# Kernel tuning notes

Hardware: AMD Instinct MI355X
Metric: run time of the kernel (lower is better)

The kernel has to match this reference:

```python
import jax, jax.numpy as jnp
import numpy as np

_INF = -1e30
EPS = 1e-8


def _masked_max(v, mask, axis, keepdims=False):
    return jnp.max(jnp.where(mask == 0, _INF, v), axis=axis, keepdims=keepdims)


def _masked_mean(v, mask, axis, keepdims=False):
    s = jnp.sum(jnp.where(mask == 0, 0.0, v), axis=axis, keepdims=keepdims)
    cnt = jnp.sum(jnp.broadcast_to(mask, v.shape), axis=axis, keepdims=keepdims)
    return s / jnp.clip(cnt, EPS, None)


def _masked_softmax(v, mask):
    return jax.nn.softmax(jnp.where(mask == 0, _INF, v), axis=-1)


def _cos(a, b, axis):
    num = jnp.sum(a * b, axis=axis)
    na = jnp.maximum(jnp.sqrt(jnp.sum(a * a, axis=axis)), EPS)
    nb = jnp.maximum(jnp.sqrt(jnp.sum(b * b, axis=axis)), EPS)
    return num / (na * nb)


def _pairwise_cos(c1, c2):
    # c1:[B,L1,H] c2:[B,L2,H] -> [B,L1,L2]
    dots = jnp.einsum('bih,bjh->bij', c1, c2)
    n1 = jnp.maximum(jnp.linalg.norm(c1, axis=-1), EPS)
    n2 = jnp.maximum(jnp.linalg.norm(c2, axis=-1), EPS)
    return dots / (n1[:, :, None] * n2[:, None, :])


def _mpm(v1, v2, w):
    # v1:[B,L,H], v2:[B,L or 1,H], w:[P,H]
    single = _cos(v1, v2, axis=2)[:, :, None]              # [B,L,1]
    wv1 = w[None, None] * v1[:, :, None, :]                # [B,L,P,H]
    wv2 = w[None, None] * v2[:, :, None, :]                # [B,Lv,P,H]
    multi = _cos(wv1, wv2, axis=3)                         # [B,L,P]
    return single, multi


def _mpm_pairwise(c1, c2, w):
    # w:[P,H] -> cosine [B,L1,L2,P]
    wv1 = w[None, :, None, :] * c1[:, None, :, :]          # [B,P,L1,H]
    wv2 = w[None, :, None, :] * c2[:, None, :, :]          # [B,P,L2,H]
    n1 = jnp.linalg.norm(wv1, axis=3, keepdims=True)       # [B,P,L1,1]
    n2 = jnp.linalg.norm(wv2, axis=3, keepdims=True)       # [B,P,L2,1]
    mul = jnp.einsum('bpih,bpjh->bpij', wv1, wv2)
    denom = jnp.clip(n1 * jnp.swapaxes(n2, 2, 3), EPS, None)
    return jnp.transpose(mul / denom, (0, 2, 3, 1))        # [B,L1,L2,P]


def _bimpm(context_1, mask_1, context_2, mask_2, w_ff, w_fb, w_mp, w_att, w_matt):
    B = context_1.shape[0]
    len1 = jnp.sum(mask_1, axis=1).astype(jnp.int32)
    len2 = jnp.sum(mask_2, axis=1).astype(jnp.int32)
    c1 = context_1 * mask_1[:, :, None]
    c2 = context_2 * mask_2[:, :, None]

    cos_sim = _pairwise_cos(c1, c2)                        # [B,L1,L2]
    m2r = mask_2[:, None, :]
    m1r = mask_1[:, None, :]
    cmax1 = _masked_max(cos_sim, m2r, 2, True)
    cmean1 = _masked_mean(cos_sim, m2r, 2, True)
    cos_t = jnp.swapaxes(cos_sim, 1, 2)
    cmax2 = _masked_max(cos_t, m1r, 2, True)
    cmean2 = _masked_mean(cos_t, m1r, 2, True)

    lp1 = jnp.clip(len1 - 1, 0, None)
    lp2 = jnp.clip(len2 - 1, 0, None)
    c1_fl = c1[jnp.arange(B), lp1][:, None, :]             # [B,1,H]
    c2_fl = c2[jnp.arange(B), lp2][:, None, :]
    c1_bl = c1[:, 0:1, :]
    c2_bl = c2[:, 0:1, :]

    mv1_ff = _mpm(c1, c2_fl, w_ff)
    mv2_ff = _mpm(c2, c1_fl, w_ff)
    mv1_bf = _mpm(c1, c2_bl, w_fb)
    mv2_bf = _mpm(c2, c1_bl, w_fb)

    mm = _mpm_pairwise(c1, c2, w_mp)                       # [B,L1,L2,P]
    mv1_max = _masked_max(mm, mask_2[:, None, :, None], 2)
    mv1_mean = _masked_mean(mm, mask_2[:, None, :, None], 2)
    mm_t = jnp.transpose(mm, (0, 2, 1, 3))
    mv2_max = _masked_max(mm_t, mask_1[:, None, :, None], 2)
    mv2_mean = _masked_mean(mm_t, mask_1[:, None, :, None], 2)

    att_2 = c2[:, None, :, :] * cos_sim[:, :, :, None]     # [B,L1,L2,H]
    att_1 = c1[:, :, None, :] * cos_sim[:, :, :, None]     # [B,L1,L2,H]
    att_mean_2 = _masked_softmax(att_2.sum(axis=2), mask_1[:, :, None])  # [B,L1,H]
    att_mean_1 = _masked_softmax(att_1.sum(axis=1), mask_2[:, :, None])  # [B,L2,H]
    mv1_am = _mpm(c1, att_mean_2, w_att)
    mv2_am = _mpm(c2, att_mean_1, w_att)

    att_max_2 = _masked_max(att_2, mask_2[:, None, :, None], 2)          # [B,L1,H]
    att_max_1 = _masked_max(jnp.transpose(att_1, (0, 2, 1, 3)), mask_1[:, None, :, None], 2)  # [B,L2,H]
    mv1_amx = _mpm(c1, att_max_2, w_matt)
    mv2_amx = _mpm(c2, att_max_1, w_matt)

    mv1 = jnp.concatenate([cmax1, cmean1, *mv1_ff, *mv1_bf, mv1_max, mv1_mean, *mv1_am, *mv1_amx], axis=-1)
    mv2 = jnp.concatenate([cmax2, cmean2, *mv2_ff, *mv2_bf, mv2_max, mv2_mean, *mv2_am, *mv2_amx], axis=-1)
    return jnp.concatenate([mv1, mv2], axis=1)             # [B, L1+L2, 102]


def setup_inputs() -> dict:
    key = jax.random.key(0)
    B, L, H, P = 8, 128, 768, 16
    ks = jax.random.split(key, 8)
    context_1 = jax.random.normal(ks[0], (B, L, H), dtype=jnp.float32)
    context_2 = jax.random.normal(ks[1], (B, L, H), dtype=jnp.float32)
    len1 = jax.random.randint(ks[2], (B,), L // 2, L + 1)
    len2 = jax.random.randint(ks[3], (B,), L // 2, L + 1)
    ar = jnp.arange(L)
    mask_1 = (ar[None, :] < len1[:, None]).astype(jnp.float32)
    mask_2 = (ar[None, :] < len2[:, None]).astype(jnp.float32)
    scale = np.sqrt(2.0 / H).astype(np.float32)
    w_ff = jax.random.normal(ks[4], (P, H), dtype=jnp.float32) * scale
    w_fb = jax.random.normal(ks[5], (P, H), dtype=jnp.float32) * scale
    w_mp = jax.random.normal(ks[6], (P, H), dtype=jnp.float32) * scale
    kk = jax.random.split(ks[7], 2)
    w_att = jax.random.normal(kk[0], (P, H), dtype=jnp.float32) * scale
    w_matt = jax.random.normal(kk[1], (P, H), dtype=jnp.float32) * scale
    return {"context_1": context_1, "mask_1": mask_1, "context_2": context_2, "mask_2": mask_2,
            "w_ff": w_ff, "w_fb": w_fb, "w_mp": w_mp, "w_att": w_att, "w_matt": w_matt}


def reference(context_1, mask_1, context_2, mask_2, w_ff, w_fb, w_mp, w_att, w_matt):
    return _bimpm(context_1, mask_1, context_2, mask_2, w_ff, w_fb, w_mp, w_att, w_matt)
```

## Files before the change

### kernel.cpp

```cpp
#include <hip/hip_runtime.h>

#define Bn 8
#define Ln 128
#define Hn 768
#define Pn 16
#define Dn 102
#define EPSF 1e-8f
#define NINF -1e30f

typedef __attribute__((ext_vector_type(8))) short bfrag8;
typedef __attribute__((ext_vector_type(4))) float f32x4;
union FragU { unsigned u[4]; bfrag8 v; };

#define MFMA16(A,B,C) __builtin_amdgcn_mfma_f32_16x16x32_bf16((A),(B),(C),0,0,0)

__device__ __forceinline__ float wred_sum(float v){
#pragma unroll
  for(int o=32;o>=1;o>>=1) v += __shfl_xor(v,o);
  return v;
}
__device__ __forceinline__ float wred_max(float v){
#pragma unroll
  for(int o=32;o>=1;o>>=1) v = fmaxf(v,__shfl_xor(v,o));
  return v;
}
__device__ __forceinline__ float qred_sum(float v){
  v += __shfl_xor(v,16);
  v += __shfl_xor(v,32);
  return v;
}

__device__ __forceinline__ void split8(const float* x, FragU& H, FragU& L){
  float r[8];
#pragma unroll
  for(int q=0;q<8;q++){
    unsigned hb = __float_as_uint(x[q]) & 0xffff0000u;
    r[q] = x[q] - __uint_as_float(hb);
  }
#pragma unroll
  for(int q=0;q<4;q++){
    H.u[q] = __builtin_amdgcn_perm(__float_as_uint(x[2*q+1]), __float_as_uint(x[2*q]), 0x07060302u);
    L.u[q] = __builtin_amdgcn_perm(__float_as_uint(r[2*q+1]), __float_as_uint(r[2*q]), 0x07060302u);
  }
}

#define GLD_LDS(gp, lp) __builtin_amdgcn_global_load_lds( \
    (const __attribute__((address_space(1))) void*)(gp), \
    (__attribute__((address_space(3))) void*)(lp), 16, 0, 0)

constexpr size_t SZ_MAT   = (size_t)Bn*Ln*Hn;
constexpr size_t OFF_C1F  = 0;
constexpr size_t OFF_C2F  = OFF_C1F + SZ_MAT;
constexpr size_t OFF_COS  = OFF_C2F + SZ_MAT;
constexpr size_t OFF_N1   = OFF_COS + (size_t)Bn*Ln*Ln;
constexpr size_t OFF_N2   = OFF_N1 + (size_t)Bn*Ln;
constexpr size_t OFF_WN   = OFF_N2 + (size_t)Bn*Ln;
constexpr size_t OFF_W2T  = OFF_WN + (size_t)2*5*Bn*Pn*Ln;
constexpr size_t OFF_MVMAX  = OFF_W2T + (size_t)5*Hn*Pn;
constexpr size_t OFF_MVMEAN = OFF_MVMAX + (size_t)2*Bn*Ln*Pn;
constexpr size_t OFF_PART   = OFF_MVMEAN + (size_t)2*Bn*Ln*Pn;
constexpr size_t OFF_LENS   = OFF_PART + (size_t)Bn*Ln*Pn*32*2;
constexpr size_t OFF_C2H    = OFF_LENS + 32;
constexpr size_t OFF_C2L    = OFF_C2H + (size_t)Bn*12*128*64/2;
constexpr size_t OFF_W2F    = OFF_C2L + (size_t)Bn*12*128*64/2;
constexpr size_t OFF_W2B    = OFF_W2F + 12288;

__device__ __forceinline__ size_t wnIdx(int side,int X,int b,int p,int i){
  return ((((size_t)side*5 + X)*Bn + b)*Pn + p)*Ln + i;
}

__global__ __launch_bounds__(256) void k_prep(
    const float* __restrict__ m1, const float* __restrict__ m2,
    const float* __restrict__ wff, const float* __restrict__ wfb,
    const float* __restrict__ wmp, const float* __restrict__ watt,
    const float* __restrict__ wmatt,
    float* __restrict__ W2T, float* __restrict__ W2F, float* __restrict__ W2B,
    int* __restrict__ lens){
  int t = threadIdx.x;
  const float* srcs[5] = {wff,wfb,wmp,watt,wmatt};
  if(blockIdx.x < 8){
    int b = blockIdx.x;
    __shared__ int cnt[2];
    if(t<2) cnt[t]=0;
    __syncthreads();
    if(t<Ln){
      if(m1[b*Ln+t]>0.5f) atomicAdd(&cnt[0],1);
      if(m2[b*Ln+t]>0.5f) atomicAdd(&cnt[1],1);
    }
    __syncthreads();
    if(t==0){
      lens[b]=cnt[0]; lens[8+b]=cnt[1];
      lens[16+b]=max(cnt[0]-1,0); lens[24+b]=max(cnt[1]-1,0);
    }
  } else if(blockIdx.x < 248){
    int idx = (blockIdx.x-8)*256 + t;
    int X = idx/(Pn*Hn);
    int r = idx%(Pn*Hn);
    int h = r/Pn, p = r%Pn;
    float w = srcs[X][p*Hn+h];
    W2T[idx] = w*w;
  } else if(blockIdx.x < 296){
    int idx = (blockIdx.x-248)*256 + t;
    int ksg = idx>>9;
    int r   = idx&511;
    int half= r>>8;
    int li  = (r>>2)&63;
    int e4  = r&3;
    int h = ksg*32 + half*16 + ((li>>4)<<2) + e4;
    int p = li&15;
    float w = wmp[p*Hn+h];
    W2F[idx] = w*w;
  } else {
    int idx = (blockIdx.x-296)*256 + t;
    int X   = idx/12288;
    int r   = idx%12288;
    int hh4 = r>>8;
    int li  = (r>>2)&63;
    int e   = r&3;
    int h = (li>>4)*192 + hh4*4 + e;
    int p = li&15;
    float w = srcs[X][p*Hn+h];
    W2B[idx] = w*w;
  }
}

__global__ __launch_bounds__(256) void k_rows(
    const float* __restrict__ ctx1, const float* __restrict__ m1,
    const float* __restrict__ ctx2, const float* __restrict__ m2,
    const float* __restrict__ W2T,
    float* __restrict__ c1f, float* __restrict__ c2f,
    unsigned short* __restrict__ c2h, unsigned short* __restrict__ c2l,
    float* __restrict__ n1, float* __restrict__ n2, float* __restrict__ wn){
  const int i0 = blockIdx.x*4, b = blockIdx.y, side = blockIdx.z;
  const float* ctx = side? ctx2 : ctx1;
  const float* msk = side? m2 : m1;
  float* dst = side? c2f : c1f;
  float* nD  = side? n2 : n1;
  const int t = threadIdx.x, w = t>>6, l = t&63;

  __shared__ float red4[4][4];
  __shared__ float redX[4][4][16];
  __shared__ float mkS[4];

  if(t<4) mkS[t] = msk[b*Ln+i0+t];

#pragma unroll
  for(int r=0;r<4;r++){
    const int i = i0+r;
    const float mk = msk[b*Ln+i];
    const size_t base = ((size_t)(b*Ln+i))*Hn;
    float ss = 0.f;
#pragma unroll
    for(int k=0;k<3;k++){
      float x = ctx[base + t + 256*k]*mk;
      dst[base + t + 256*k] = x;
      ss = fmaf(x,x,ss);
      if(side==1){
        int h = t+256*k;
        int kc = h>>6, hw = h&63, u = hw>>2, e = hw&3;
        int pos = ((u ^ (i&15))<<2) + e;
        size_t o = ((size_t)(b*12+kc)*128 + i)*64 + pos;
        unsigned hb = __float_as_uint(x) & 0xffff0000u;
        float rem = x - __uint_as_float(hb);
        c2h[o] = (unsigned short)(hb>>16);
        c2l[o] = (unsigned short)(__float_as_uint(rem)>>16);
      }
    }
    ss = wred_sum(ss);
    if(l==0) red4[r][w]=ss;
  }
  __syncthreads();
  if(t<4) nD[b*Ln+i0+t] = sqrtf(fmaxf(red4[t][0]+red4[t][1]+red4[t][2]+red4[t][3],0.f));

  const int pq = t&3, hc = t>>2;
  const int h0 = hc*12;
  float v2r[4][12];
#pragma unroll
  for(int r=0;r<4;r++){
    const float mk = mkS[r];
    const float* src = ctx + ((size_t)(b*Ln+i0+r))*Hn + h0;
#pragma unroll
    for(int q=0;q<3;q++){
      float4 xv = *(const float4*)(src + q*4);
      v2r[r][q*4+0]=xv.x*xv.x*mk; v2r[r][q*4+1]=xv.y*xv.y*mk;
      v2r[r][q*4+2]=xv.z*xv.z*mk; v2r[r][q*4+3]=xv.w*xv.w*mk;
    }
  }
  for(int X=0;X<5;++X){
    float acc[4][4];
#pragma unroll
    for(int r=0;r<4;r++){ acc[r][0]=0.f; acc[r][1]=0.f; acc[r][2]=0.f; acc[r][3]=0.f; }
    const float* wb = W2T + (size_t)X*Hn*Pn + pq*4;
#pragma unroll
    for(int h=0;h<12;h++){
      float4 w4 = *(const float4*)(wb + (size_t)(h0+h)*Pn);
#pragma unroll
      for(int r=0;r<4;r++){
        acc[r][0]=fmaf(w4.x,v2r[r][h],acc[r][0]);
        acc[r][1]=fmaf(w4.y,v2r[r][h],acc[r][1]);
        acc[r][2]=fmaf(w4.z,v2r[r][h],acc[r][2]);
        acc[r][3]=fmaf(w4.w,v2r[r][h],acc[r][3]);
      }
    }
#pragma unroll
    for(int r=0;r<4;r++)
#pragma unroll
      for(int pi=0;pi<4;pi++){
        float v = acc[r][pi];
        v += __shfl_xor(v,4); v += __shfl_xor(v,8);
        v += __shfl_xor(v,16); v += __shfl_xor(v,32);
        acc[r][pi]=v;
      }
    if(l<4){
#pragma unroll
      for(int r=0;r<4;r++)
#pragma unroll
        for(int pi=0;pi<4;pi++) redX[w][l][r*4+pi]=acc[r][pi];
    }
    __syncthreads();
    if(t<64){
      int r = t>>4, p = t&15;
      int pqi = p>>2, pii = p&3;
      float s = redX[0][pqi][r*4+pii]+redX[1][pqi][r*4+pii]
               +redX[2][pqi][r*4+pii]+redX[3][pqi][r*4+pii];
      wn[wnIdx(side,X,b,p,i0+r)] = s;
    }
    __syncthreads();
  }
}

__global__ __launch_bounds__(512) void k_mm(
    const float* __restrict__ c1f,
    const unsigned short* __restrict__ c2h, const unsigned short* __restrict__ c2l,
    const float* __restrict__ W2F, const float* __restrict__ WN,
    const float* __restrict__ n1, const float* __restrict__ n2,
    const float* __restrict__ m1, const float* __restrict__ m2,
    const int* __restrict__ lens,
    float* __restrict__ cosM,
    float* __restrict__ mvmax, float* __restrict__ mvmean,
    float* __restrict__ part){
  const int b = blockIdx.x, ig = blockIdx.y, ibase = ig*4;
  const int t = threadIdx.x, l = t&63;
  const int wid = __builtin_amdgcn_readfirstlane(t>>6);
  const int jtp = wid&3, ihalf = wid>>2;
  const int p = l&15, g4 = l>>4;

  __shared__ __align__(16) unsigned short sB2h[2][128][64];
  __shared__ __align__(16) unsigned short sB2l[2][128][64];
  __shared__ __align__(16) float sw2[2][1024];
  __shared__ __align__(16) float sa[2][4][64];
  __shared__ float sm2s[Ln];
  __shared__ float red0[2][4][2][16][2];

  const size_t c2elem = (size_t)b*12*8192;

  {
#pragma unroll
    for(int k=0;k<2;k++){
      GLD_LDS((const char*)c2h + c2elem*2 + (2*wid+k)*1024 + l*16,
              (char*)&sB2h[0][0][0] + (2*wid+k)*1024);
      GLD_LDS((const char*)c2l + c2elem*2 + (2*wid+k)*1024 + l*16,
              (char*)&sB2l[0][0][0] + (2*wid+k)*1024);
    }
    if(wid>=4){
      int q = wid-4;
      GLD_LDS((const char*)W2F + q*1024 + l*16,
              (char*)&sw2[0][0] + q*1024);
    }
    if(t<Ln) sm2s[t] = m2[b*Ln+t];
    if(t<64){
      int row = t>>4, u = t&15;
      float4 av = *(const float4*)(c1f + ((size_t)(b*Ln+ibase+row))*Hn + u*4);
      *(float4*)&sa[0][row][(u ^ (row&3))<<2] = av;
    }
  }
  __syncthreads();

  f32x4 accE[2][2]; f32x4 accC[2];
#pragma unroll
  for(int q=0;q<2;q++){
    accC[q] = (f32x4){0.f,0.f,0.f,0.f};
#pragma unroll
    for(int ii=0;ii<2;ii++) accE[q][ii] = (f32x4){0.f,0.f,0.f,0.f};
  }

  for(int c=0; c<12; ++c){
    const int cur = c&1, nxt = cur^1;
    const bool more = (c+1<12);
    float4 aN;
    if(more){
      const size_t cb2 = (c2elem + (size_t)(c+1)*8192)*2;
#pragma unroll
      for(int k=0;k<2;k++){
        GLD_LDS((const char*)c2h + cb2 + (2*wid+k)*1024 + l*16,
                (char*)&sB2h[nxt][0][0] + (2*wid+k)*1024);
        GLD_LDS((const char*)c2l + cb2 + (2*wid+k)*1024 + l*16,
                (char*)&sB2l[nxt][0][0] + (2*wid+k)*1024);
      }
      if(wid>=4){
        int q = wid-4;
        GLD_LDS((const char*)W2F + (c+1)*4096 + q*1024 + l*16,
                (char*)&sw2[nxt][0] + q*1024);
      }
      if(t<64){
        int row = t>>4, u = t&15;
        aN = *(const float4*)(c1f + ((size_t)(b*Ln+ibase+row))*Hn + (c+1)*64 + u*4);
      }
    }
#pragma unroll
    for(int ks=0; ks<2; ++ks){
      f32x4 w20 = *(const f32x4*)&sw2[cur][(ks*2+0)*256 + (l<<2)];
      f32x4 w21 = *(const f32x4*)&sw2[cur][(ks*2+1)*256 + (l<<2)];
      FragU Bh[2], Bl[2];
#pragma unroll
      for(int q=0;q<2;q++){
        int jt = jtp + 4*q;
        int j  = jt*16 + p;
        const char* bh = (const char*)&sB2h[cur][0][0] + j*128;
        const char* bl = (const char*)&sB2l[cur][0][0] + j*128;
        int u1 = (ks*8 + g4)     ^ (j&15);
        int u2 = (ks*8 + 4 + g4) ^ (j&15);
        uint2 h0 = *(const uint2*)(bh + (u1<<3));
        uint2 h1 = *(const uint2*)(bh + (u2<<3));
        uint2 l0 = *(const uint2*)(bl + (u1<<3));
        uint2 l1 = *(const uint2*)(bl + (u2<<3));
        Bh[q].u[0]=h0.x; Bh[q].u[1]=h0.y; Bh[q].u[2]=h1.x; Bh[q].u[3]=h1.y;
        Bl[q].u[0]=l0.x; Bl[q].u[1]=l0.y; Bl[q].u[2]=l1.x; Bl[q].u[3]=l1.y;
      }
      if(ihalf==0){
        int ar = p&3;
        const float* sar = &sa[cur][ar][0];
        f32x4 a0 = *(const f32x4*)(sar + (((ks*8+g4)  ^ar)<<2));
        f32x4 a1 = *(const f32x4*)(sar + (((ks*8+4+g4)^ar)<<2));
        float xv[8] = {a0[0],a0[1],a0[2],a0[3], a1[0],a1[1],a1[2],a1[3]};
        FragU Ah, Al; split8(xv, Ah, Al);
#pragma unroll
        for(int q=0;q<2;q++){
          accC[q] = MFMA16(Bh[q].v, Ah.v, accC[q]);
          accC[q] = MFMA16(Bh[q].v, Al.v, accC[q]);
          accC[q] = MFMA16(Bl[q].v, Ah.v, accC[q]);
        }
      }
#pragma unroll
      for(int ii=0;ii<2;ii++){
        int row = ihalf*2+ii;
        const float* sar = &sa[cur][row][0];
        f32x4 a0 = *(const f32x4*)(sar + (((ks*8+g4)  ^(row&3))<<2));
        f32x4 a1 = *(const f32x4*)(sar + (((ks*8+4+g4)^(row&3))<<2));
        float xv[8] = {a0[0]*w20[0], a0[1]*w20[1], a0[2]*w20[2], a0[3]*w20[3],
                       a1[0]*w21[0], a1[1]*w21[1], a1[2]*w21[2], a1[3]*w21[3]};
        FragU Ah, Al; split8(xv, Ah, Al);
#pragma unroll
        for(int q=0;q<2;q++){
          accE[q][ii] = MFMA16(Bh[q].v, Ah.v, accE[q][ii]);
          accE[q][ii] = MFMA16(Bh[q].v, Al.v, accE[q][ii]);
          accE[q][ii] = MFMA16(Bl[q].v, Ah.v, accE[q][ii]);
        }
      }
    }
    if(more && t<64){
      int row = t>>4, u = t&15;
      *(float4*)&sa[nxt][row][(u ^ (row&3))<<2] = aN;
    }
    __syncthreads();
  }

  const int len2 = min(max(lens[8+b],1),Ln);
  float sq1[2][4];
#pragma unroll
  for(int q=0;q<2;q++){
    int jt = jtp+4*q;
#pragma unroll
    for(int r=0;r<4;r++){
      int j = jt*16 + g4*4 + r;
      sq1[q][r] = sqrtf(fmaxf(WN[wnIdx(1,2,b,p,j)],0.f));
    }
  }
  float s1M[2][4], s1S[2][4];
#pragma unroll
  for(int q=0;q<2;q++)
#pragma unroll
    for(int r=0;r<4;r++){ s1M[q][r]=NINF; s1S[q][r]=0.f; }

#pragma unroll
  for(int ii=0;ii<2;ii++){
    int iR = ibase + ihalf*2 + ii;
    float sr = sqrtf(fmaxf(WN[wnIdx(0,2,b,p,iR)],0.f));
    float mr = m1[b*Ln+iR];
    float vmax=NINF, vsum=0.f;
#pragma unroll
    for(int q=0;q<2;q++){
      int jt = jtp+4*q;
#pragma unroll
      for(int r=0;r<4;r++){
        int j = jt*16 + g4*4 + r;
        float ev = accE[q][ii][r] / fmaxf(sr*sq1[q][r], EPSF);
        if(sm2s[j]!=0.f){ vmax=fmaxf(vmax,ev); vsum+=ev; }
        if(mr!=0.f){ s1M[q][r]=fmaxf(s1M[q][r],ev); s1S[q][r]+=ev; }
      }
    }
    vmax = fmaxf(vmax, __shfl_xor(vmax,16)); vmax = fmaxf(vmax, __shfl_xor(vmax,32));
    vsum += __shfl_xor(vsum,16); vsum += __shfl_xor(vsum,32);
    if(l<16){ red0[ihalf][jtp][ii][l][0]=vmax; red0[ihalf][jtp][ii][l][1]=vsum; }
  }
  float* red1 = (float*)&sB2h[0][0][0];
  if(ihalf==1){
#pragma unroll
    for(int q=0;q<2;q++)
#pragma unroll
      for(int r=0;r<4;r++){
        int idx = (((jtp*2+q)*64 + l)*4 + r)*2;
        red1[idx]   = s1M[q][r];
        red1[idx+1] = s1S[q][r];
      }
  }
  __syncthreads();
  if(t<64){
    int ih_=t>>5, ii_=(t>>4)&1, p_=t&15;
    float M=NINF,S=0.f;
#pragma unroll
    for(int jq=0;jq<4;jq++){ M=fmaxf(M,red0[ih_][jq][ii_][p_][0]); S+=red0[ih_][jq][ii_][p_][1]; }
    int iR = ibase + ih_*2 + ii_;
    size_t o = ((size_t)(b*Ln+iR))*Pn + p_;
    mvmax[o]=M; mvmean[o]=S/(float)len2;
  }
  if(ihalf==0){
#pragma unroll
    for(int q=0;q<2;q++){
      int jt = jtp+4*q;
#pragma unroll
      for(int r=0;r<4;r++){
        int j = jt*16 + g4*4 + r;
        int idx = (((jtp*2+q)*64 + l)*4 + r)*2;
        float M = fmaxf(s1M[q][r], red1[idx]);
        float S = s1S[q][r] + red1[idx+1];
        size_t o = ((((size_t)(b*Ln+j))*Pn + p)*32 + ig)*2;
        part[o]=M; part[o+1]=S;
        float nj = fmaxf(n2[b*Ln+j], EPSF);
        if(p<4){
          int iR = ibase + p;
          float ni = fmaxf(n1[b*Ln+iR], EPSF);
          cosM[((size_t)(b*Ln+iR))*Ln + j] = accC[q][r]/(ni*nj);
        }
      }
    }
  }
}

__global__ __launch_bounds__(256) void k_mm2(
    const float* __restrict__ part, const int* __restrict__ lens,
    float* __restrict__ mvmax, float* __restrict__ mvmean){
  int g = blockIdx.x*256 + threadIdx.x;
  int b = g>>11;
  const float4* q = (const float4*)(part + (size_t)g*64);
  float mx = NINF, sm = 0.f;
#pragma unroll
  for(int k=0;k<16;k++){
    float4 v = q[k];
    mx = fmaxf(mx, fmaxf(v.x, v.z));
    sm += v.y + v.w;
  }
  int len1 = min(max(lens[b],1),Ln);
  size_t o = (size_t)Bn*Ln*Pn + g;
  mvmax[o] = mx;
  mvmean[o] = sm/(float)len1;
}

#define HPAD 784
__global__ __launch_bounds__(256) void k_fin(
    const float* __restrict__ c1f, const float* __restrict__ c2f,
    const float* __restrict__ cosM,
    const float* __restrict__ n1, const float* __restrict__ n2,
    const float* __restrict__ wn, const float* __restrict__ W2B,
    const float* __restrict__ mvmax, const float* __restrict__ mvmean,
    const int* __restrict__ lens,
    const float* __restrict__ m1, const float* __restrict__ m2,
    float* __restrict__ out){
  const int x = blockIdx.x, side = x>>3, b = x&7;
  const int r0 = blockIdx.y*4;
  const int t = threadIdx.x, w = t>>6, l = t&63;
  const float* selfF  = side? c2f : c1f;
  const float* otherF = side? c1f : c2f;
  const float* nSelf  = side? n2 : n1;
  const float* nOther = side? n1 : n2;
  const float* mInner = side? m1 : m2;
  const float* mSelfm = side? m2 : m1;
  int lenI = side? lens[b]    : lens[8+b];
  int lpO  = side? lens[16+b] : lens[24+b];
  lenI = min(max(lenI,1),Ln);
  lpO  = min(max(lpO,0),Ln-1);

  __shared__ float cS[4*Ln];
  __shared__ float mS[Ln];
  __shared__ __align__(16) float sV1[4][HPAD];
  __shared__ __align__(16) float sF[HPAD], sB[HPAD];
  __shared__ __align__(16) float sAS[4][HPAD], sAM[4][HPAD];
  __shared__ float redm[4][4], reds[4][4];

  {
    if(side==0){
      const float* crow = cosM + ((size_t)(b*Ln+r0))*Ln;
      for(int idx=t; idx<4*Ln; idx+=256) cS[idx]=crow[idx];
    } else {
      for(int idx=t; idx<4*Ln; idx+=256){
        int jj = idx&127, rp = idx>>7;
        cS[rp*Ln+jj] = cosM[((size_t)(b*Ln+jj))*Ln + r0+rp];
      }
    }
    if(t<Ln) mS[t]=mInner[b*Ln+t];
    const float4* s4 = (const float4*)(selfF + ((size_t)(b*Ln+r0))*Hn);
    for(int idx=t; idx<4*Hn/4; idx+=256){
      int row = idx/192, q = idx - row*192;
      ((float4*)&sV1[row][0])[q + q/48] = s4[idx];
    }
    const float4* f4 = (const float4*)(otherF + ((size_t)(b*Ln+lpO))*Hn);
    const float4* b4 = (const float4*)(otherF + ((size_t)(b*Ln))*Hn);
    if(t<Hn/4){
      ((float4*)sF)[t + t/48]=f4[t];
      ((float4*)sB)[t + t/48]=b4[t];
    }
  }
  __syncthreads();

  float aS[4][3], aM[4][3];
#pragma unroll
  for(int r=0;r<4;r++)
#pragma unroll
    for(int k=0;k<3;k++){ aS[r][k]=0.f; aM[r][k]=NINF; }
  {
    const float* src = otherF + (size_t)b*Ln*Hn;
#pragma unroll 2
    for(int jj=0; jj<lenI; ++jj){
      float3 vk = ((const float3*)(src + (size_t)jj*Hn))[t];
      float c0=cS[jj], c1v=cS[Ln+jj], c2v=cS[2*Ln+jj], c3v=cS[3*Ln+jj];
      aS[0][0]=fmaf(vk.x,c0 ,aS[0][0]); aS[0][1]=fmaf(vk.y,c0 ,aS[0][1]); aS[0][2]=fmaf(vk.z,c0 ,aS[0][2]);
      aS[1][0]=fmaf(vk.x,c1v,aS[1][0]); aS[1][1]=fmaf(vk.y,c1v,aS[1][1]); aS[1][2]=fmaf(vk.z,c1v,aS[1][2]);
      aS[2][0]=fmaf(vk.x,c2v,aS[2][0]); aS[2][1]=fmaf(vk.y,c2v,aS[2][1]); aS[2][2]=fmaf(vk.z,c2v,aS[2][2]);
      aS[3][0]=fmaf(vk.x,c3v,aS[3][0]); aS[3][1]=fmaf(vk.y,c3v,aS[3][1]); aS[3][2]=fmaf(vk.z,c3v,aS[3][2]);
      aM[0][0]=fmaxf(aM[0][0],vk.x*c0 ); aM[0][1]=fmaxf(aM[0][1],vk.y*c0 ); aM[0][2]=fmaxf(aM[0][2],vk.z*c0 );
      aM[1][0]=fmaxf(aM[1][0],vk.x*c1v); aM[1][1]=fmaxf(aM[1][1],vk.y*c1v); aM[1][2]=fmaxf(aM[1][2],vk.z*c1v);
      aM[2][0]=fmaxf(aM[2][0],vk.x*c2v); aM[2][1]=fmaxf(aM[2][1],vk.y*c2v); aM[2][2]=fmaxf(aM[2][2],vk.z*c2v);
      aM[3][0]=fmaxf(aM[3][0],vk.x*c3v); aM[3][1]=fmaxf(aM[3][1],vk.y*c3v); aM[3][2]=fmaxf(aM[3][2],vk.z*c3v);
    }
  }

  {
#pragma unroll
    for(int r=0;r<4;r++){
      float lm = fmaxf(fmaxf(aS[r][0],aS[r][1]),aS[r][2]);
      lm = wred_max(lm);
      if(l==0) redm[r][w]=lm;
    }
  }
  __syncthreads();
  float bm[4];
#pragma unroll
  for(int r=0;r<4;r++)
    bm[r] = fmaxf(fmaxf(redm[r][0],redm[r][1]),fmaxf(redm[r][2],redm[r][3]));
  float ev[4][3];
  {
#pragma unroll
    for(int r=0;r<4;r++){
      float es=0.f;
#pragma unroll
      for(int k=0;k<3;k++){ ev[r][k]=expf(aS[r][k]-bm[r]); es+=ev[r][k]; }
      es = wred_sum(es);
      if(l==0) reds[r][w]=es;
    }
  }
  __syncthreads();
  {
    const float u = 1.f/(float)Hn;
#pragma unroll
    for(int r=0;r<4;r++){
      float smr = mSelfm[b*Ln+r0+r];
      float bs = reds[r][0]+reds[r][1]+reds[r][2]+reds[r][3];
      float inv = 1.f/fmaxf(bs,EPSF);
#pragma unroll
      for(int k=0;k<3;k++){
        int h = 3*t+k;
        int hi = h + ((h/192)<<2);
        sAS[r][hi] = (smr!=0.f)? ev[r][k]*inv : u;
        sAM[r][hi] = aM[r][k];
      }
    }
  }
  __syncthreads();

  {
    int rr = w;
    float cmx=NINF, csm=0.f;
    float ca = cS[rr*Ln + l], cb = cS[rr*Ln + l + 64];
    if(mS[l]!=0.f){ cmx=ca; csm=ca; }
    if(mS[l+64]!=0.f){ cmx=fmaxf(cmx,cb); csm+=cb; }
    cmx = wred_max(cmx); csm = wred_sum(csm);
    if(l==0){
      float* op = out + ((size_t)((b*2+side)*Ln + r0+rr))*Dn;
      op[0] = cmx;
      op[1] = csm/(float)lenI;
    }
  }
  if(t<128){
    int rr = t>>5, qq = t&31, p = qq&15;
    size_t o = ((size_t)((side*Bn+b)*Ln + r0+rr))*Pn + p;
    float* op = out + ((size_t)((b*2+side)*Ln + r0+rr))*Dn;
    if(qq<16) op[36+p] = mvmax[o];
    else      op[52+p] = mvmean[o];
  }

  {
    const int Xids[4] = {0,1,3,4};
    const int offS[4] = {2,19,68,85};
    const int X = Xids[w], offs = offS[w];
    const bool dyn = (w>=2);
    const int p = l&15, hq = l>>4;
    const int hb = hq*196;
    const float4* wB = (const float4*)W2B + (size_t)X*3072 + l;
    float acc[4]={0,0,0,0}, s0[4]={0,0,0,0};
    float sna[4]={0,0,0,0}, sn[4]={0,0,0,0};
    if(!dyn){
      const float* bvp = (w==0)? sF : sB;
#pragma unroll 4
      for(int h4=0; h4<48; ++h4){
        float4 w4 = wB[h4*64];
        float4 bv = *(const float4*)(bvp + hb + h4*4);
#pragma unroll
        for(int r=0;r<4;r++){
          float4 v = *(const float4*)(&sV1[r][hb + h4*4]);
          float pr;
          pr=v.x*bv.x; acc[r]=fmaf(w4.x,pr,acc[r]); s0[r]+=pr;
          pr=v.y*bv.y; acc[r]=fmaf(w4.y,pr,acc[r]); s0[r]+=pr;
          pr=v.z*bv.z; acc[r]=fmaf(w4.z,pr,acc[r]); s0[r]+=pr;
          pr=v.w*bv.w; acc[r]=fmaf(w4.w,pr,acc[r]); s0[r]+=pr;
        }
      }
    } else {
      const float (*bvp)[HPAD] = (w==2)? sAS : sAM;
#pragma unroll 2
      for(int h4=0; h4<48; ++h4){
        float4 w4 = wB[h4*64];
#pragma unroll
        for(int r=0;r<4;r++){
          float4 bv = *(const float4*)(&bvp[r][hb + h4*4]);
          float4 v  = *(const float4*)(&sV1[r][hb + h4*4]);
          float pr, bb;
          pr=v.x*bv.x; bb=bv.x*bv.x;
          acc[r]=fmaf(w4.x,pr,acc[r]); sna[r]=fmaf(w4.x,bb,sna[r]); s0[r]+=pr; sn[r]+=bb;
          pr=v.y*bv.y; bb=bv.y*bv.y;
          acc[r]=fmaf(w4.y,pr,acc[r]); sna[r]=fmaf(w4.y,bb,sna[r]); s0[r]+=pr; sn[r]+=bb;
          pr=v.z*bv.z; bb=bv.z*bv.z;
          acc[r]=fmaf(w4.z,pr,acc[r]); sna[r]=fmaf(w4.z,bb,sna[r]); s0[r]+=pr; sn[r]+=bb;
          pr=v.w*bv.w; bb=bv.w*bv.w;
          acc[r]=fmaf(w4.w,pr,acc[r]); sna[r]=fmaf(w4.w,bb,sna[r]); s0[r]+=pr; sn[r]+=bb;
        }
      }
    }
#pragma unroll
    for(int r=0;r<4;r++){
      acc[r]=qred_sum(acc[r]); s0[r]=qred_sum(s0[r]);
      if(dyn){ sna[r]=qred_sum(sna[r]); sn[r]=qred_sum(sn[r]); }
    }
#pragma unroll
    for(int rr=0; rr<4; ++rr){
      const int r = r0+rr;
      float* op = out + ((size_t)((b*2+side)*Ln + r))*Dn;
      if(l<16){
        float wa = fmaxf(wn[wnIdx(side,X,b,l,r)],0.f);
        float wb = dyn? fmaxf(sna[rr],0.f)
                      : fmaxf(wn[wnIdx(1-side,X,b,l,(w==0? lpO:0))],0.f);
        float mul = acc[rr]/(fmaxf(sqrtf(wa),EPSF)*fmaxf(sqrtf(wb),EPSF));
        op[offs+1+l] = mul;
      }
      if(l==0){
        float nb = dyn? sqrtf(fmaxf(sn[rr],0.f)) : nOther[b*Ln + (w==0? lpO : 0)];
        float nv1 = nSelf[b*Ln+r];
        op[offs] = s0[rr]/(fmaxf(nv1,EPSF)*fmaxf(nb,EPSF));
      }
    }
  }
}

extern "C" void kernel_launch(void* const* d_in, const int* in_sizes, int n_in,
                              void* d_out, int out_size, void* d_ws, size_t ws_size,
                              hipStream_t stream) {
  const float* ctx1 = (const float*)d_in[0];
  const float* m1   = (const float*)d_in[1];
  const float* ctx2 = (const float*)d_in[2];
  const float* m2   = (const float*)d_in[3];
  const float* wff  = (const float*)d_in[4];
  const float* wfb  = (const float*)d_in[5];
  const float* wmp  = (const float*)d_in[6];
  const float* watt = (const float*)d_in[7];
  const float* wmatt= (const float*)d_in[8];
  float* out = (float*)d_out;
  float* W = (float*)d_ws;
  int* lens = (int*)(W + OFF_LENS);
  unsigned short* c2h = (unsigned short*)(W + OFF_C2H);
  unsigned short* c2l = (unsigned short*)(W + OFF_C2L);

  k_prep<<<dim3(8 + 240 + 48 + 240), 256, 0, stream>>>(m1,m2,wff,wfb,wmp,watt,wmatt,
      W+OFF_W2T, W+OFF_W2F, W+OFF_W2B, lens);
  k_rows<<<dim3(Ln/4,Bn,2), 256, 0, stream>>>(ctx1,m1,ctx2,m2, W+OFF_W2T,
      W+OFF_C1F, W+OFF_C2F, c2h, c2l, W+OFF_N1, W+OFF_N2, W+OFF_WN);
  k_mm<<<dim3(Bn, 32), 512, 0, stream>>>(W+OFF_C1F, c2h, c2l,
      W+OFF_W2F, W+OFF_WN, W+OFF_N1, W+OFF_N2, m1, m2, lens,
      W+OFF_COS, W+OFF_MVMAX, W+OFF_MVMEAN, W+OFF_PART);
  k_mm2<<<dim3((Bn*Ln*Pn)/256), 256, 0, stream>>>(W+OFF_PART, lens,
      W+OFF_MVMAX, W+OFF_MVMEAN);
  k_fin<<<dim3(16, Ln/4), 256, 0, stream>>>(W+OFF_C1F, W+OFF_C2F, W+OFF_COS,
      W+OFF_N1, W+OFF_N2, W+OFF_WN, W+OFF_W2B, W+OFF_MVMAX, W+OFF_MVMEAN,
      lens, m1, m2, out);
}
```

Measured before the change: 160.9 us.

## Split k_fin attention accumulation across two thread halves with 512-thread blocks

Doubles k_fin's block size to 512 threads. The two halves each accumulate over half of the inner sequence for the attentive sum and max, then combine partial results through a new shared scratch buffer. The later multi-perspective stage splits the four rows across the two halves, two rows per wave. This aims to cut the serial loop length per thread and raise parallelism in the final kernel, at the cost of more shared memory (about 25 KB extra), an extra barrier, and an idle half during the softmax phase.

```diff
diff --git a/kernel.cpp b/kernel.cpp
--- a/kernel.cpp
+++ b/kernel.cpp
@@ -467,7 +467,7 @@
 }
 
 #define HPAD 784
-__global__ __launch_bounds__(256) void k_fin(
+__global__ __launch_bounds__(512) void k_fin(
     const float* __restrict__ c1f, const float* __restrict__ c2f,
     const float* __restrict__ cosM,
     const float* __restrict__ n1, const float* __restrict__ n2,
@@ -479,6 +479,7 @@
   const int x = blockIdx.x, side = x>>3, b = x&7;
   const int r0 = blockIdx.y*4;
   const int t = threadIdx.x, w = t>>6, l = t&63;
+  const int jh = t>>8, tt = t&255;
   const float* selfF  = side? c2f : c1f;
   const float* otherF = side? c1f : c2f;
   const float* nSelf  = side? n2 : n1;
@@ -495,21 +496,22 @@
   __shared__ __align__(16) float sV1[4][HPAD];
   __shared__ __align__(16) float sF[HPAD], sB[HPAD];
   __shared__ __align__(16) float sAS[4][HPAD], sAM[4][HPAD];
+  __shared__ float scr[256*25];
   __shared__ float redm[4][4], reds[4][4];
 
   {
     if(side==0){
       const float* crow = cosM + ((size_t)(b*Ln+r0))*Ln;
-      for(int idx=t; idx<4*Ln; idx+=256) cS[idx]=crow[idx];
+      for(int idx=t; idx<4*Ln; idx+=512) cS[idx]=crow[idx];
     } else {
-      for(int idx=t; idx<4*Ln; idx+=256){
+      for(int idx=t; idx<4*Ln; idx+=512){
         int jj = idx&127, rp = idx>>7;
         cS[rp*Ln+jj] = cosM[((size_t)(b*Ln+jj))*Ln + r0+rp];
       }
     }
     if(t<Ln) mS[t]=mInner[b*Ln+t];
     const float4* s4 = (const float4*)(selfF + ((size_t)(b*Ln+r0))*Hn);
-    for(int idx=t; idx<4*Hn/4; idx+=256){
+    for(int idx=t; idx<4*Hn/4; idx+=512){
       int row = idx/192, q = idx - row*192;
       ((float4*)&sV1[row][0])[q + q/48] = s4[idx];
     }
@@ -528,10 +530,13 @@
 #pragma unroll
     for(int k=0;k<3;k++){ aS[r][k]=0.f; aM[r][k]=NINF; }
   {
+    const int half = (lenI+1)>>1;
+    const int jbeg = jh? half : 0;
+    const int jend = jh? lenI : half;
     const float* src = otherF + (size_t)b*Ln*Hn;
 #pragma unroll 2
-    for(int jj=0; jj<lenI; ++jj){
-      float3 vk = ((const float3*)(src + (size_t)jj*Hn))[t];
+    for(int jj=jbeg; jj<jend; ++jj){
+      float3 vk = ((const float3*)(src + (size_t)jj*Hn))[tt];
       float c0=cS[jj], c1v=cS[Ln+jj], c2v=cS[2*Ln+jj], c3v=cS[3*Ln+jj];
       aS[0][0]=fmaf(vk.x,c0 ,aS[0][0]); aS[0][1]=fmaf(vk.y,c0 ,aS[0][1]); aS[0][2]=fmaf(vk.z,c0 ,aS[0][2]);
       aS[1][0]=fmaf(vk.x,c1v,aS[1][0]); aS[1][1]=fmaf(vk.y,c1v,aS[1][1]); aS[1][2]=fmaf(vk.z,c1v,aS[1][2]);
@@ -543,8 +548,26 @@
       aM[3][0]=fmaxf(aM[3][0],vk.x*c3v); aM[3][1]=fmaxf(aM[3][1],vk.y*c3v); aM[3][2]=fmaxf(aM[3][2],vk.z*c3v);
     }
   }
-
-  {
+  if(jh==1){
+    float* sp = scr + tt*25;
+#pragma unroll
+    for(int r=0;r<4;r++)
+#pragma unroll
+      for(int k=0;k<3;k++){ sp[r*6+k*2]=aS[r][k]; sp[r*6+k*2+1]=aM[r][k]; }
+  }
+  __syncthreads();
+  if(jh==0){
+    const float* sp = scr + tt*25;
+#pragma unroll
+    for(int r=0;r<4;r++)
+#pragma unroll
+      for(int k=0;k<3;k++){
+        aS[r][k] += sp[r*6+k*2];
+        aM[r][k] = fmaxf(aM[r][k], sp[r*6+k*2+1]);
+      }
+  }
+
+  if(jh==0){
 #pragma unroll
     for(int r=0;r<4;r++){
       float lm = fmaxf(fmaxf(aS[r][0],aS[r][1]),aS[r][2]);
@@ -553,12 +576,12 @@
     }
   }
   __syncthreads();
-  float bm[4];
-#pragma unroll
-  for(int r=0;r<4;r++)
-    bm[r] = fmaxf(fmaxf(redm[r][0],redm[r][1]),fmaxf(redm[r][2],redm[r][3]));
-  float ev[4][3];
-  {
+  if(jh==0){
+    float bm[4];
+#pragma unroll
+    for(int r=0;r<4;r++)
+      bm[r] = fmaxf(fmaxf(redm[r][0],redm[r][1]),fmaxf(redm[r][2],redm[r][3]));
+    float ev[4][3];
 #pragma unroll
     for(int r=0;r<4;r++){
       float es=0.f;
@@ -566,10 +589,11 @@
       for(int k=0;k<3;k++){ ev[r][k]=expf(aS[r][k]-bm[r]); es+=ev[r][k]; }
       es = wred_sum(es);
       if(l==0) reds[r][w]=es;
+      aS[r][0]=ev[r][0]; aS[r][1]=ev[r][1]; aS[r][2]=ev[r][2];
     }
   }
   __syncthreads();
-  {
+  if(jh==0){
     const float u = 1.f/(float)Hn;
 #pragma unroll
     for(int r=0;r<4;r++){
@@ -578,16 +602,16 @@
       float inv = 1.f/fmaxf(bs,EPSF);
 #pragma unroll
       for(int k=0;k<3;k++){
-        int h = 3*t+k;
+        int h = 3*tt+k;
         int hi = h + ((h/192)<<2);
-        sAS[r][hi] = (smr!=0.f)? ev[r][k]*inv : u;
+        sAS[r][hi] = (smr!=0.f)? aS[r][k]*inv : u;
         sAM[r][hi] = aM[r][k];
       }
     }
   }
   __syncthreads();
 
-  {
+  if(w<4){
     int rr = w;
     float cmx=NINF, csm=0.f;
     float ca = cS[rr*Ln + l], cb = cS[rr*Ln + l + 64];
@@ -599,9 +623,9 @@
       op[0] = cmx;
       op[1] = csm/(float)lenI;
     }
-  }
-  if(t<128){
-    int rr = t>>5, qq = t&31, p = qq&15;
+  } else if(t>=256 && t<384){
+    int q = t-256;
+    int rr = q>>5, qq = q&31, p = qq&15;
     size_t o = ((size_t)((side*Bn+b)*Ln + r0+rr))*Pn + p;
     float* op = out + ((size_t)((b*2+side)*Ln + r0+rr))*Dn;
     if(qq<16) op[36+p] = mvmax[o];
@@ -611,22 +635,22 @@
   {
     const int Xids[4] = {0,1,3,4};
     const int offS[4] = {2,19,68,85};
-    const int X = Xids[w], offs = offS[w];
-    const bool dyn = (w>=2);
+    const int X = Xids[w&3], offs = offS[w&3];
+    const bool dyn = ((w&3)>=2);
+    const int rp = (w>>2)*2;
     const int p = l&15, hq = l>>4;
     const int hb = hq*196;
     const float4* wB = (const float4*)W2B + (size_t)X*3072 + l;
-    float acc[4]={0,0,0,0}, s0[4]={0,0,0,0};
-    float sna[4]={0,0,0,0}, sn[4]={0,0,0,0};
+    float acc[2]={0,0}, s0[2]={0,0}, sna[2]={0,0}, sn[2]={0,0};
     if(!dyn){
-      const float* bvp = (w==0)? sF : sB;
+      const float* bvp = ((w&3)==0)? sF : sB;
 #pragma unroll 4
       for(int h4=0; h4<48; ++h4){
         float4 w4 = wB[h4*64];
         float4 bv = *(const float4*)(bvp + hb + h4*4);
 #pragma unroll
-        for(int r=0;r<4;r++){
-          float4 v = *(const float4*)(&sV1[r][hb + h4*4]);
+        for(int r=0;r<2;r++){
+          float4 v = *(const float4*)(&sV1[rp+r][hb + h4*4]);
           float pr;
           pr=v.x*bv.x; acc[r]=fmaf(w4.x,pr,acc[r]); s0[r]+=pr;
           pr=v.y*bv.y; acc[r]=fmaf(w4.y,pr,acc[r]); s0[r]+=pr;
@@ -635,14 +659,14 @@
         }
       }
     } else {
-      const float (*bvp)[HPAD] = (w==2)? sAS : sAM;
-#pragma unroll 2
+      const float (*bvp)[HPAD] = ((w&3)==2)? sAS : sAM;
+#pragma unroll 4
       for(int h4=0; h4<48; ++h4){
         float4 w4 = wB[h4*64];
 #pragma unroll
-        for(int r=0;r<4;r++){
-          float4 bv = *(const float4*)(&bvp[r][hb + h4*4]);
-          float4 v  = *(const float4*)(&sV1[r][hb + h4*4]);
+        for(int r=0;r<2;r++){
+          float4 bv = *(const float4*)(&bvp[rp+r][hb + h4*4]);
+          float4 v  = *(const float4*)(&sV1[rp+r][hb + h4*4]);
           float pr, bb;
           pr=v.x*bv.x; bb=bv.x*bv.x;
           acc[r]=fmaf(w4.x,pr,acc[r]); sna[r]=fmaf(w4.x,bb,sna[r]); s0[r]+=pr; sn[r]+=bb;
@@ -656,23 +680,23 @@
       }
     }
 #pragma unroll
-    for(int r=0;r<4;r++){
+    for(int r=0;r<2;r++){
       acc[r]=qred_sum(acc[r]); s0[r]=qred_sum(s0[r]);
       if(dyn){ sna[r]=qred_sum(sna[r]); sn[r]=qred_sum(sn[r]); }
     }
 #pragma unroll
-    for(int rr=0; rr<4; ++rr){
-      const int r = r0+rr;
+    for(int rr=0; rr<2; ++rr){
+      const int r = r0 + rp + rr;
       float* op = out + ((size_t)((b*2+side)*Ln + r))*Dn;
       if(l<16){
         float wa = fmaxf(wn[wnIdx(side,X,b,l,r)],0.f);
         float wb = dyn? fmaxf(sna[rr],0.f)
-                      : fmaxf(wn[wnIdx(1-side,X,b,l,(w==0? lpO:0))],0.f);
+                      : fmaxf(wn[wnIdx(1-side,X,b,l,((w&3)==0? lpO:0))],0.f);
         float mul = acc[rr]/(fmaxf(sqrtf(wa),EPSF)*fmaxf(sqrtf(wb),EPSF));
         op[offs+1+l] = mul;
       }
       if(l==0){
-        float nb = dyn? sqrtf(fmaxf(sn[rr],0.f)) : nOther[b*Ln + (w==0? lpO : 0)];
+        float nb = dyn? sqrtf(fmaxf(sn[rr],0.f)) : nOther[b*Ln + ((w&3)==0? lpO : 0)];
         float nv1 = nSelf[b*Ln+r];
         op[offs] = s0[rr]/(fmaxf(nv1,EPSF)*fmaxf(nb,EPSF));
       }
@@ -707,7 +731,7 @@
       W+OFF_COS, W+OFF_MVMAX, W+OFF_MVMEAN, W+OFF_PART);
   k_mm2<<<dim3((Bn*Ln*Pn)/256), 256, 0, stream>>>(W+OFF_PART, lens,
       W+OFF_MVMAX, W+OFF_MVMEAN);
-  k_fin<<<dim3(16, Ln/4), 256, 0, stream>>>(W+OFF_C1F, W+OFF_C2F, W+OFF_COS,
+  k_fin<<<dim3(16, Ln/4), 512, 0, stream>>>(W+OFF_C1F, W+OFF_C2F, W+OFF_COS,
       W+OFF_N1, W+OFF_N2, W+OFF_WN, W+OFF_W2B, W+OFF_MVMAX, W+OFF_MVMEAN,
       lens, m1, m2, out);
 }
```

Result: slower. 170.9 us (+6.2%).
